# Kernel tuning notes

Hardware: AMD Instinct MI355X
Metric: run time of the kernel (lower is better)

## Reference

```python
import jax, jax.numpy as jnp
import numpy as np

B, S, D, H, DH, FF = 2, 2048, 1024, 16, 64, 4096
EPS = 1e-6


def setup_inputs() -> dict:
    key = jax.random.key(0)
    ks = jax.random.split(key, 12)
    s = lambda fan: 1.0 / np.sqrt(fan)
    return {
        "x": jax.random.normal(ks[0], (B, S, D), dtype=jnp.float32),
        "mask": jax.random.randint(ks[1], (B, S), 0, 2).astype(bool),
        "Wq": jax.random.normal(ks[2], (D, H * DH), dtype=jnp.float32) * s(D),
        "Wk": jax.random.normal(ks[3], (D, H * DH), dtype=jnp.float32) * s(D),
        "Wv": jax.random.normal(ks[4], (D, H * DH), dtype=jnp.float32) * s(D),
        "Wo": jax.random.normal(ks[5], (H * DH, D), dtype=jnp.float32) * s(H * DH),
        "bo": jnp.zeros((D,), dtype=jnp.float32),
        "W1": jax.random.normal(ks[6], (D, FF), dtype=jnp.float32) * s(D),
        "b1": jnp.zeros((FF,), dtype=jnp.float32),
        "W2": jax.random.normal(ks[7], (FF, D), dtype=jnp.float32) * s(FF),
        "b2": jnp.zeros((D,), dtype=jnp.float32),
        "g1": jnp.ones((D,), dtype=jnp.float32),   # layer_norm1 target_std
        "m1": jnp.zeros((D,), dtype=jnp.float32),  # layer_norm1 target_mean
        "g2": jnp.ones((D,), dtype=jnp.float32),
        "m2": jnp.zeros((D,), dtype=jnp.float32),
    }


def layer_norm(x, g, m):
    mu = jnp.mean(x, axis=-1, keepdims=True)
    xc = x - mu
    std = jnp.sqrt(jnp.mean(xc * xc, axis=-1, keepdims=True) + EPS)
    return g * xc / std + m


def reference(x, mask, Wq, Wk, Wv, Wo, bo, W1, b1, W2, b2, g1, m1, g2, m2):
    # --- multi-head self-attention (no proj bias) ---
    q = (x @ Wq).reshape(B, S, H, DH)
    k = (x @ Wk).reshape(B, S, H, DH)
    v = (x @ Wv).reshape(B, S, H, DH)
    scores = jnp.einsum("bqhd,bkhd->bhqk", q, k) / np.sqrt(DH)  # [B,H,S,S]
    scores = jnp.where(mask[:, None, None, :], -jnp.inf, scores)
    att = jax.nn.softmax(scores, axis=-1)
    ctx = jnp.einsum("bhqk,bkhd->bqhd", att, v).reshape(B, S, H * DH)
    attn_out = ctx @ Wo + bo
    # --- post-LN residual block (pre_ln=False, dropouts=0 in eval) ---
    x1 = layer_norm(attn_out + x, g1, m1)
    ff = jax.nn.relu(x1 @ W1 + b1) @ W2 + b2
    return layer_norm(ff + x1, g2, m2)
```

## Files before the change

kernel.cpp:

```cpp
#include <hip/hip_runtime.h>
#include <hip/hip_bf16.h>


typedef __bf16 bf16;
typedef __bf16 bf16x8 __attribute__((ext_vector_type(8)));
typedef __bf16 bf16x4 __attribute__((ext_vector_type(4)));
typedef float  f32x4  __attribute__((ext_vector_type(4)));
typedef float  f32x16 __attribute__((ext_vector_type(16)));
typedef unsigned u32x2 __attribute__((ext_vector_type(2)));
typedef unsigned u32x4 __attribute__((ext_vector_type(4)));

#define DEVI __device__ __forceinline__

constexpr int S_LEN  = 2048;
constexpr int NTOK   = 4096;
constexpr int DMODEL = 1024;
constexpr int NFF    = 4096;
constexpr float SCALE2 = 0.125f * 1.44269504088896f;
constexpr float MASKV2 = -30000.0f;

DEVI void gld16(const void* g, void* l) {
  __builtin_amdgcn_global_load_lds((const __attribute__((address_space(1))) void*)g,
                                   (__attribute__((address_space(3))) void*)l, 16, 0, 0);
}

DEVI f32x4 mfma16(bf16x8 a, bf16x8 b, f32x4 c) {
  return __builtin_amdgcn_mfma_f32_16x16x32_bf16(a, b, c, 0, 0, 0);
}
DEVI f32x16 mfma32(bf16x8 a, bf16x8 b, f32x16 c) {
  return __builtin_amdgcn_mfma_f32_32x32x16_bf16(a, b, c, 0, 0, 0);
}
DEVI unsigned cvtpk(float lo, float hi) {
  unsigned d;
  asm("v_cvt_pk_bf16_f32 %0, %1, %2" : "=v"(d) : "v"(lo), "v"(hi));
  return d;
}
DEVI void plswap(unsigned &a, unsigned &b) {
#if __has_builtin(__builtin_amdgcn_permlane32_swap)
  u32x2 r = __builtin_amdgcn_permlane32_swap(a, b, false, false);
  a = r[0]; b = r[1];
#else
  asm volatile("v_permlane32_swap_b32 %0, %1" : "+v"(a), "+v"(b));
#endif
}
DEVI float fexp2(float x) {
#if __has_builtin(__builtin_amdgcn_exp2f)
  return __builtin_amdgcn_exp2f(x);
#else
  return exp2f(x);
#endif
}
#define M3(a, b, c) fmaxf(fmaxf(a, b), c)

template <int MODE>
__global__ __launch_bounds__(256) void gemm_bt(
    const bf16* __restrict__ A, const bf16* __restrict__ Bt,
    void* __restrict__ out, const float* __restrict__ bias,
    int M, int N, int ld, int Kc, int nx, int ny)
{
  __shared__ bf16 As[128 * 32];
  __shared__ bf16 Bs[128 * 32];
  const int tid  = threadIdx.x;
  const int lane = tid & 63, w = tid >> 6;
  const int wr = w >> 1, wc = w & 1;

  const int id  = blockIdx.x;
  const int xcd = id & 7;
  int t2 = id >> 3;
  const int bx = t2 % nx;  t2 /= nx;
  const int ppx = ny >> 3;
  const int kz = t2 / ppx;
  const int by = xcd * ppx + (t2 % ppx);
  const int brow = by * 128, bcol = bx * 128;

  const bf16* Ag = A  + (size_t)(brow + w * 32 + (lane >> 2)) * ld + kz * Kc + (lane & 3) * 8;
  const bf16* Bg = Bt + (size_t)(bcol + w * 32 + (lane >> 2)) * ld + kz * Kc + (lane & 3) * 8;
  bf16* AsW = As + w * 1024;
  bf16* BsW = Bs + w * 1024;

  f32x4 acc[4][4] = {};

  for (int k0 = 0; k0 < Kc; k0 += 32) {
    gld16(Ag + k0,                    AsW);
    gld16(Ag + k0 + (size_t)16 * ld,  AsW + 512);
    gld16(Bg + k0,                    BsW);
    gld16(Bg + k0 + (size_t)16 * ld,  BsW + 512);
    __syncthreads();

    bf16x8 af[4], bfr[4];
#pragma unroll
    for (int m = 0; m < 4; ++m)
      af[m] = *(const bf16x8*)&As[(wr * 64 + m * 16 + (lane & 15)) * 32 + (lane >> 4) * 8];
#pragma unroll
    for (int n = 0; n < 4; ++n)
      bfr[n] = *(const bf16x8*)&Bs[(wc * 64 + n * 16 + (lane & 15)) * 32 + (lane >> 4) * 8];
    __builtin_amdgcn_s_setprio(1);
#pragma unroll
    for (int m = 0; m < 4; ++m)
#pragma unroll
      for (int n = 0; n < 4; ++n)
        acc[m][n] = mfma16(af[m], bfr[n], acc[m][n]);
    __builtin_amdgcn_s_setprio(0);
    __syncthreads();
  }

  const size_t plane = (size_t)NTOK * DMODEL;
#pragma unroll
  for (int m = 0; m < 4; ++m)
#pragma unroll
    for (int n = 0; n < 4; ++n)
#pragma unroll
      for (int r = 0; r < 4; ++r) {
        const int row = brow + wr * 64 + m * 16 + (lane >> 4) * 4 + r;
        const int col = bcol + wc * 64 + n * 16 + (lane & 15);
        const float v = acc[m][n][r];
        if (MODE == 0) {
          const int b = row >> 11, s = row & 2047;
          const int which = col >> 10, c = col & 1023, h = c >> 6, d = c & 63;
          bf16* qkv = (bf16*)out;
          if (which == 0)
            qkv[(((size_t)(b * 16 + h)) * 2048 + s) * 64 + d] = (bf16)(v * SCALE2);
          else if (which == 1)
            (qkv + plane)[(((size_t)(b * 16 + h)) * 2048 + s) * 64 + d] = (bf16)v;
          else
            (qkv + 2 * plane)[(((size_t)(b * 16 + h)) * 64 + d) * 2048 + s] = (bf16)v;
        } else if (MODE == 3) {
          const float t = v + bias[col];
          ((bf16*)out)[(size_t)row * N + col] = (bf16)fmaxf(t, 0.0f);
        } else {
          ((float*)out)[(size_t)kz * M * N + (size_t)row * N + col] = v;
        }
      }
}

__global__ __launch_bounds__(512) void attn_k(
    const bf16* __restrict__ q, const bf16* __restrict__ k,
    const bf16* __restrict__ vt, const unsigned* __restrict__ mbits,
    bf16* __restrict__ ctx)
{
  __shared__ __align__(16) char smem[36864];
  bf16* Kl = (bf16*)smem;
  bf16* Vl = (bf16*)(smem + 16384);
  const int tid = threadIdx.x, lane = tid & 63, w = tid >> 6;
  const int hi = lane >> 5, li = lane & 31;
  const int id = blockIdx.x;
  const int j = id >> 3;
  const int bh = (id & 7) * 4 + (j & 3);
  const int b = bh >> 4, h = bh & 15;
  const int qbase = (j >> 2) * 256 + w * 32;

  bf16x8 qf[4];
  {
    const bf16* qp = q + ((size_t)bh * S_LEN + qbase + li) * 64 + hi * 8;
#pragma unroll
    for (int c = 0; c < 4; ++c) qf[c] = *(const bf16x8*)(qp + c * 16);
  }
  const u32x4 onesu = {0x3F803F80u, 0x3F803F80u, 0x3F803F80u, 0x3F803F80u};
  const bf16x8 onesv = __builtin_bit_cast(bf16x8, onesu);

  f32x16 o[2] = {};
  f32x16 acc1 = {};
  float mrun = -3.0e38f;

  const int srow = w * 8 + (lane >> 3);
  const int sslot = (lane & 7) ^ ((srow ^ (srow >> 3)) & 7);
  const bf16* kg = k  + ((size_t)bh * S_LEN + srow) * 64 + sslot * 8;
  const bf16* vg = vt + ((size_t)bh * 64 + srow) * S_LEN + sslot * 8;

  gld16(kg, Kl + w * 512);
  gld16(vg, Vl + w * 512);
  __syncthreads();

  int buf = 0;
  for (int kt = 0; kt < 32; ++kt) {
    const int nb = buf ^ 1;
    if (kt + 1 < 32) {
      gld16(kg + (size_t)(kt + 1) * 4096, Kl + nb * 4096 + w * 512);
      gld16(vg + (kt + 1) * 64,           Vl + nb * 4096 + w * 512);
    }
    const unsigned mw0 = mbits[b * 64 + kt * 2]     >> (hi * 4);
    const unsigned mw1 = mbits[b * 64 + kt * 2 + 1] >> (hi * 4);
    const bf16* Kb = Kl + buf * 4096;
    const bf16* Vb = Vl + buf * 4096;

    float sc[2][16];
#pragma unroll
    for (int kblk = 0; kblk < 2; ++kblk) {
      const int key = kblk * 32 + li;
      const unsigned swb = ((key ^ (key >> 3)) & 7) << 4;
      const char* kr = (const char*)Kb + key * 128;
      f32x16 st = {};
      __builtin_amdgcn_s_setprio(1);
#pragma unroll
      for (int c = 0; c < 4; ++c) {
        const bf16x8 kf = *(const bf16x8*)(kr + ((unsigned)(c * 32 + hi * 16) ^ swb));
        st = mfma32(kf, qf[c], st);
      }
      __builtin_amdgcn_s_setprio(0);
      const unsigned msh = kblk ? mw1 : mw0;
#pragma unroll
      for (int r = 0; r < 16; ++r) {
        const int cb = (r & 3) + 8 * (r >> 2);
        sc[kblk][r] = (msh & (1u << cb)) ? MASKV2 : st[r];
      }
    }

    const float* sf = &sc[0][0];
    float m0[11];
#pragma unroll
    for (int i3 = 0; i3 < 10; ++i3) m0[i3] = M3(sf[i3 * 3], sf[i3 * 3 + 1], sf[i3 * 3 + 2]);
    m0[10] = fmaxf(sf[30], sf[31]);
    float tm = fmaxf(fmaxf(M3(m0[0], m0[1], m0[2]), M3(m0[3], m0[4], m0[5])),
                     fmaxf(M3(m0[6], m0[7], m0[8]), fmaxf(m0[9], m0[10])));
    tm = fmaxf(tm, __shfl_xor(tm, 32, 64));

    if (!__all(tm <= mrun + 11.0f)) {
      const float mnew = fmaxf(mrun, tm);
      const float alpha = fexp2(mrun - mnew);
      mrun = mnew;
      o[0] *= alpha;
      o[1] *= alpha;
      acc1[0] = acc1[0] * alpha;
    }
#pragma unroll
    for (int kblk = 0; kblk < 2; ++kblk)
#pragma unroll
      for (int r = 0; r < 16; ++r)
        sc[kblk][r] = fexp2(sc[kblk][r] - mrun);

    bf16x8 pa[4];
#pragma unroll
    for (int kblk = 0; kblk < 2; ++kblk)
#pragma unroll
      for (int hf = 0; hf < 2; ++hf) {
        unsigned A = cvtpk(sc[kblk][hf * 8 + 0], sc[kblk][hf * 8 + 1]);
        unsigned B = cvtpk(sc[kblk][hf * 8 + 2], sc[kblk][hf * 8 + 3]);
        unsigned C = cvtpk(sc[kblk][hf * 8 + 4], sc[kblk][hf * 8 + 5]);
        unsigned D = cvtpk(sc[kblk][hf * 8 + 6], sc[kblk][hf * 8 + 7]);
        plswap(A, C);
        plswap(B, D);
        const u32x4 t = {A, B, C, D};
        pa[kblk * 2 + hf] = __builtin_bit_cast(bf16x8, t);
      }

#pragma unroll
    for (int dblk = 0; dblk < 2; ++dblk) {
      const int d = dblk * 32 + li;
      const unsigned swb = ((d ^ (d >> 3)) & 7) << 4;
      const char* vr = (const char*)Vb + d * 128;
      __builtin_amdgcn_s_setprio(1);
#pragma unroll
      for (int ch = 0; ch < 4; ++ch) {
        const bf16x8 vf = *(const bf16x8*)(vr + ((unsigned)(ch * 32 + hi * 16) ^ swb));
        o[dblk] = mfma32(vf, pa[ch], o[dblk]);
      }
      __builtin_amdgcn_s_setprio(0);
    }
#pragma unroll
    for (int ch = 0; ch < 4; ++ch) acc1 = mfma32(onesv, pa[ch], acc1);
    __syncthreads();
    buf = nb;
  }

  const float rl = 1.0f / acc1[0];
  char* Ep = smem + w * 4608;
#pragma unroll
  for (int dblk = 0; dblk < 2; ++dblk)
#pragma unroll
    for (int g = 0; g < 4; ++g) {
      const unsigned lo = cvtpk(o[dblk][4 * g + 0] * rl, o[dblk][4 * g + 1] * rl);
      const unsigned hw = cvtpk(o[dblk][4 * g + 2] * rl, o[dblk][4 * g + 3] * rl);
      const int d0 = 8 * g + 4 * hi + 32 * dblk;
      *(unsigned long long*)(Ep + li * 144 + d0 * 2) =
          ((unsigned long long)hw << 32) | (unsigned long long)lo;
    }
#pragma unroll
  for (int i = 0; i < 4; ++i) {
    const int r = (lane >> 3) + 8 * i;
    const bf16x8 vv = *(const bf16x8*)(Ep + r * 144 + (lane & 7) * 16);
    *(bf16x8*)(ctx + ((size_t)b * S_LEN + qbase + r) * DMODEL + h * 64 + (lane & 7) * 8) = vv;
  }
}

template <int NPART, int RB>
__global__ __launch_bounds__(256) void ln_k(
    const float* __restrict__ parts, const float* __restrict__ bias,
    const void* __restrict__ resid, const float* __restrict__ gam,
    const float* __restrict__ bet, float* __restrict__ of, bf16* __restrict__ ob)
{
  const int row = blockIdx.x, t = threadIdx.x;
  float4 v = ((const float4*)(parts + (size_t)row * DMODEL))[t];
#pragma unroll
  for (int p = 1; p < NPART; ++p) {
    const float4 u = ((const float4*)(parts + ((size_t)p * NTOK + row) * DMODEL))[t];
    v.x += u.x; v.y += u.y; v.z += u.z; v.w += u.w;
  }
  {
    const float4 b4 = ((const float4*)bias)[t];
    float4 r4;
    if (RB) {
      const bf16x4 rb = *(const bf16x4*)((const bf16*)resid + (size_t)row * DMODEL + t * 4);
      r4.x = (float)rb[0]; r4.y = (float)rb[1]; r4.z = (float)rb[2]; r4.w = (float)rb[3];
    } else {
      r4 = ((const float4*)((const float*)resid + (size_t)row * DMODEL))[t];
    }
    v.x += b4.x + r4.x; v.y += b4.y + r4.y; v.z += b4.z + r4.z; v.w += b4.w + r4.w;
  }
  float s  = v.x + v.y + v.z + v.w;
  float s2 = v.x * v.x + v.y * v.y + v.z * v.z + v.w * v.w;
#pragma unroll
  for (int off = 1; off < 64; off <<= 1) {
    s  += __shfl_xor(s, off, 64);
    s2 += __shfl_xor(s2, off, 64);
  }
  __shared__ float ps[4], ps2[4];
  if ((t & 63) == 0) { ps[t >> 6] = s; ps2[t >> 6] = s2; }
  __syncthreads();
  s  = ps[0] + ps[1] + ps[2] + ps[3];
  s2 = ps2[0] + ps2[1] + ps2[2] + ps2[3];
  const float mu   = s * (1.f / 1024.f);
  const float var  = fmaxf(s2 * (1.f / 1024.f) - mu * mu, 0.f);
  const float rstd = rsqrtf(var + 1e-6f);
  const float4 g4 = ((const float4*)gam)[t];
  const float4 b4 = ((const float4*)bet)[t];
  float4 ov;
  ov.x = g4.x * (v.x - mu) * rstd + b4.x;
  ov.y = g4.y * (v.y - mu) * rstd + b4.y;
  ov.z = g4.z * (v.z - mu) * rstd + b4.z;
  ov.w = g4.w * (v.w - mu) * rstd + b4.w;
  if (of) ((float4*)(of + (size_t)row * DMODEL))[t] = ov;
  if (ob) {
    const bf16x4 o4 = {(bf16)ov.x, (bf16)ov.y, (bf16)ov.z, (bf16)ov.w};
    *(bf16x4*)(ob + (size_t)row * DMODEL + t * 4) = o4;
  }
}

__global__ __launch_bounds__(256) void prep_k(
    const float* __restrict__ x, const float* __restrict__ Wq,
    const float* __restrict__ Wk, const float* __restrict__ Wv,
    const float* __restrict__ Wo, const float* __restrict__ W1,
    const float* __restrict__ W2, const void* __restrict__ mask,
    bf16* __restrict__ xb, bf16* __restrict__ WqkvT, bf16* __restrict__ WoT,
    bf16* __restrict__ W1T, bf16* __restrict__ W2T, unsigned* __restrict__ mbits)
{
  __shared__ float tile[32][33];
  __shared__ int s_gt1, s_f1;
  const int tid = threadIdx.x;
  const int id = blockIdx.x;

  if (id < 4096) {
    const int i = id * 256 + tid;
    const float4 v = ((const float4*)x)[i];
    const bf16x4 o = {(bf16)v.x, (bf16)v.y, (bf16)v.z, (bf16)v.w};
    *(bf16x4*)(xb + (size_t)i * 4) = o;
    return;
  }
  if (id == 16384) {
    if (tid == 0) { s_gt1 = 0; s_f1 = 0; }
    __syncthreads();
    const unsigned* wds = (const unsigned*)mask;
    int gt1 = 0, f1 = 0;
    for (int i = tid; i < 1024; i += 256) {
      const unsigned xw = wds[i];
      gt1 |= (xw > 1u);
      f1  |= (xw == 0x3F800000u);
    }
    if (gt1) atomicOr(&s_gt1, 1);
    if (f1)  atomicOr(&s_f1, 1);
    __syncthreads();
    const int md = s_f1 ? 2 : (s_gt1 ? 1 : 0);
    if (tid < NTOK / 32) {
      unsigned wd = 0;
      for (int jj = 0; jj < 32; ++jj) {
        const int e = tid * 32 + jj;
        unsigned mv;
        if (md == 1)      mv = (((const unsigned char*)mask)[e] != 0);
        else if (md == 2) mv = (((const float*)mask)[e] != 0.f);
        else              mv = (((const int*)mask)[e] != 0);
        wd |= mv << jj;
      }
      mbits[tid] = wd;
    }
    return;
  }
  const float* src; bf16* dst; int K, N, bx, by;
  if (id < 7168) {
    int s2 = id - 4096; const int wq = s2 >> 10; s2 &= 1023;
    src = wq == 0 ? Wq : (wq == 1 ? Wk : Wv);
    dst = WqkvT + (size_t)wq * DMODEL * DMODEL;
    K = 1024; N = 1024; bx = s2 & 31; by = s2 >> 5;
  } else if (id < 8192) {
    const int s2 = id - 7168;
    src = Wo; dst = WoT; K = 1024; N = 1024; bx = s2 & 31; by = s2 >> 5;
  } else if (id < 12288) {
    const int s2 = id - 8192;
    src = W1; dst = W1T; K = 1024; N = 4096; bx = s2 & 127; by = s2 >> 7;
  } else {
    const int s2 = id - 12288;
    src = W2; dst = W2T; K = 4096; N = 1024; bx = s2 & 31; by = s2 >> 5;
  }
  const int tx = tid & 31, ty = tid >> 5;
  const int r0 = by * 32, c0 = bx * 32;
#pragma unroll
  for (int i = 0; i < 32; i += 8)
    tile[ty + i][tx] = src[(size_t)(r0 + ty + i) * N + c0 + tx];
  __syncthreads();
#pragma unroll
  for (int i = 0; i < 32; i += 8)
    dst[(size_t)(c0 + ty + i) * K + r0 + tx] = (bf16)tile[tx][ty + i];
}

extern "C" void kernel_launch(void* const* d_in, const int* in_sizes, int n_in,
                              void* d_out, int out_size, void* d_ws, size_t ws_size,
                              hipStream_t stream)
{
  const float* x    = (const float*)d_in[0];
  const void*  mask = d_in[1];
  const float* Wq   = (const float*)d_in[2];
  const float* Wk   = (const float*)d_in[3];
  const float* Wv   = (const float*)d_in[4];
  const float* Wo   = (const float*)d_in[5];
  const float* bo   = (const float*)d_in[6];
  const float* W1   = (const float*)d_in[7];
  const float* b1   = (const float*)d_in[8];
  const float* W2   = (const float*)d_in[9];
  const float* b2   = (const float*)d_in[10];
  const float* g1   = (const float*)d_in[11];
  const float* m1   = (const float*)d_in[12];
  const float* g2   = (const float*)d_in[13];
  const float* m2   = (const float*)d_in[14];

  const size_t plane = (size_t)NTOK * DMODEL;

  char* ws = (char*)d_ws;
  size_t off = 0;
  auto alloc = [&](size_t bytes) {
    char* p = ws + off;
    off += (bytes + 255) & ~(size_t)255;
    return p;
  };
  bf16* xb     = (bf16*)alloc(plane * 2);
  bf16* WqkvT  = (bf16*)alloc((size_t)3 * DMODEL * DMODEL * 2);
  bf16* WoT    = (bf16*)alloc((size_t)DMODEL * DMODEL * 2);
  bf16* W1T    = (bf16*)alloc((size_t)NFF * DMODEL * 2);
  bf16* W2T    = (bf16*)alloc((size_t)DMODEL * NFF * 2);
  bf16* qkv    = (bf16*)alloc(4 * plane * 2);
  bf16* qb = qkv, *kb = qkv + plane, *vtb = qkv + 2 * plane, *ctxb = qkv + 3 * plane;
  bf16* hb     = qkv;
  float* parts = (float*)alloc(2 * plane * 4);
  bf16*  x1b   = (bf16*)alloc(plane * 2);
  unsigned* maskbits = (unsigned*)alloc(512);

  prep_k<<<dim3(16385), dim3(256), 0, stream>>>(
      x, Wq, Wk, Wv, Wo, W1, W2, mask, xb, WqkvT, WoT, W1T, W2T, maskbits);

  gemm_bt<0><<<dim3(768), dim3(256), 0, stream>>>(
      xb, WqkvT, qkv, nullptr, NTOK, 3 * DMODEL, DMODEL, DMODEL, 24, 32);

  attn_k<<<dim3(256), dim3(512), 0, stream>>>(qb, kb, vtb, maskbits, ctxb);

  gemm_bt<4><<<dim3(512), dim3(256), 0, stream>>>(
      ctxb, WoT, parts, nullptr, NTOK, DMODEL, DMODEL, DMODEL / 2, 8, 32);
  ln_k<2, 0><<<dim3(NTOK), dim3(256), 0, stream>>>(parts, bo, x, g1, m1, nullptr, x1b);

  gemm_bt<3><<<dim3(1024), dim3(256), 0, stream>>>(
      x1b, W1T, hb, b1, NTOK, NFF, DMODEL, DMODEL, 32, 32);
  gemm_bt<4><<<dim3(512), dim3(256), 0, stream>>>(
      hb, W2T, parts, nullptr, NTOK, DMODEL, NFF, NFF / 2, 8, 32);
  ln_k<2, 1><<<dim3(NTOK), dim3(256), 0, stream>>>(parts, b2, x1b, g2, m2, (float*)d_out, nullptr);
}
```

Measured before the change: 271.9 us.

## Add 256x256 eight-wave pipelined GEMM for QKV and FFN1 projections

Adds a new GEMM kernel with 256x256 block tiles, 512 threads, and a 64-wide K step. It double-buffers LDS through direct global-to-LDS loads, swizzles LDS to avoid bank conflicts, and splits each K step into eight phases that interleave the next stage's loads with MFMA work, using explicit vmcnt waits and barriers. The kernel replaces the 128x128 gemm_bt for the QKV projection and the W1+ReLU projection. This targets more reuse per tile and hidden load latency, but uses 128KB of LDS, which limits occupancy to one block per CU. The QKV launch has only 192 blocks, which may leave some CUs idle.

```diff
diff --git a/kernel.cpp b/kernel.cpp
--- a/kernel.cpp
+++ b/kernel.cpp
@@ -51,6 +51,134 @@
 #endif
 }
 #define M3(a, b, c) fmaxf(fmaxf(a, b), c)
+
+template <int MODE>
+__global__ __launch_bounds__(512) void gemm8p(
+    const bf16* __restrict__ A, const bf16* __restrict__ Bt,
+    void* __restrict__ out, const float* __restrict__ bias, int N, int nx)
+{
+  __shared__ bf16 lds8[65536];
+  const int tid = threadIdx.x, lane = tid & 63, w = tid >> 6;
+  const int wr = w >> 2, wc = w & 3;
+  const int li16 = lane & 15, hi4 = lane >> 4, l7 = lane & 7, b3 = (lane >> 3) & 1;
+
+  const int id = blockIdx.x;
+  const int t2 = id >> 3;
+  const int bx = t2 % nx;
+  const int by = (id & 7) * 2 + t2 / nx;
+  const int brow = by * 256, bcol = bx * 256;
+
+  const int srow = tid >> 3;
+  const int ssl  = (tid & 7) ^ ((srow ^ (srow >> 3)) & 7);
+  const bf16* aG = A  + ((size_t)(brow + srow)) * 1024 + ssl * 8;
+  const bf16* bG = Bt + ((size_t)(bcol + srow)) * 1024 + ssl * 8;
+
+  auto STA = [&](int buf, int t, int h) {
+    const bf16* g = aG + t * 64 + (size_t)(h * 2) * 65536;
+    gld16(g,         lds8 + buf * 32768 + (h * 2) * 4096 + w * 512);
+    gld16(g + 65536, lds8 + buf * 32768 + (h * 2 + 1) * 4096 + w * 512);
+  };
+  auto STB = [&](int buf, int t, int h) {
+    const bf16* g = bG + t * 64 + (size_t)(h * 2) * 65536;
+    gld16(g,         lds8 + buf * 32768 + 16384 + (h * 2) * 4096 + w * 512);
+    gld16(g + 65536, lds8 + buf * 32768 + 16384 + (h * 2 + 1) * 4096 + w * 512);
+  };
+
+  const int sa[4] = { l7 ^ ((0 + b3) & 7), l7 ^ ((2 + b3) & 7),
+                      l7 ^ ((4 + b3) & 7), l7 ^ ((6 + b3) & 7) };
+  const int sb[2] = { l7 ^ ((wc * 4 + 0 + b3) & 7), l7 ^ ((wc * 4 + 2 + b3) & 7) };
+
+  f32x4 acc[2][2][4][2] = {};
+
+#define VM4 asm volatile("s_waitcnt vmcnt(4)" ::: "memory")
+#define VM0 asm volatile("s_waitcnt vmcnt(0)" ::: "memory")
+#define NOP ((void)0)
+#define PH(BUF, MQ, NQ, STG, WAIT) do {                                          \
+    bf16x8 af[4][2], bg[2][2];                                                   \
+    _Pragma("unroll") for (int m = 0; m < 4; ++m) {                              \
+      const bf16* rp = lds8 + (BUF) * 32768 +                                    \
+                       ((MQ) * 128 + wr * 64 + m * 16 + li16) * 64;              \
+      _Pragma("unroll") for (int ks = 0; ks < 2; ++ks)                           \
+        af[m][ks] = *(const bf16x8*)(rp + ((ks * 4 + hi4) ^ sa[m]) * 8);         \
+    }                                                                            \
+    _Pragma("unroll") for (int n = 0; n < 2; ++n) {                              \
+      const bf16* rp = lds8 + (BUF) * 32768 + 16384 +                            \
+                       ((NQ) * 128 + wc * 32 + n * 16 + li16) * 64;              \
+      _Pragma("unroll") for (int ks = 0; ks < 2; ++ks)                           \
+        bg[n][ks] = *(const bf16x8*)(rp + ((ks * 4 + hi4) ^ sb[n]) * 8);         \
+    }                                                                            \
+    STG;                                                                         \
+    asm volatile("s_barrier" ::: "memory");                                      \
+    __builtin_amdgcn_s_setprio(1);                                               \
+    _Pragma("unroll") for (int m = 0; m < 4; ++m)                                \
+      _Pragma("unroll") for (int n = 0; n < 2; ++n)                              \
+        _Pragma("unroll") for (int ks = 0; ks < 2; ++ks)                         \
+          acc[MQ][NQ][m][n] = mfma16(af[m][ks], bg[n][ks], acc[MQ][NQ][m][n]);   \
+    __builtin_amdgcn_s_setprio(0);                                               \
+    __builtin_amdgcn_sched_barrier(0);                                           \
+    WAIT;                                                                        \
+    asm volatile("s_barrier" ::: "memory");                                      \
+  } while (0)
+
+  STA(0, 0, 0); STA(0, 0, 1); STB(0, 0, 0); STB(0, 0, 1);
+  STA(1, 1, 0); STB(1, 1, 0);
+  VM4;
+  asm volatile("s_barrier" ::: "memory");
+
+  for (int it = 0; it < 7; ++it) {
+    const int t = 2 * it;
+    PH(0, 0, 0, STA(1, t + 1, 1), NOP);
+    PH(0, 0, 1, STB(1, t + 1, 1), NOP);
+    PH(0, 1, 0, STA(0, t + 2, 0), NOP);
+    PH(0, 1, 1, STB(0, t + 2, 0), VM4);
+    PH(1, 0, 0, STA(0, t + 2, 1), NOP);
+    PH(1, 0, 1, STB(0, t + 2, 1), NOP);
+    PH(1, 1, 0, STA(1, t + 3, 0), NOP);
+    PH(1, 1, 1, STB(1, t + 3, 0), VM4);
+  }
+  PH(0, 0, 0, STA(1, 15, 1), NOP);
+  PH(0, 0, 1, STB(1, 15, 1), NOP);
+  PH(0, 1, 0, NOP, NOP);
+  PH(0, 1, 1, NOP, VM0);
+  PH(1, 0, 0, NOP, NOP);
+  PH(1, 0, 1, NOP, NOP);
+  PH(1, 1, 0, NOP, NOP);
+  PH(1, 1, 1, NOP, NOP);
+#undef PH
+#undef VM4
+#undef VM0
+#undef NOP
+
+  const size_t plane = (size_t)NTOK * DMODEL;
+#pragma unroll
+  for (int mq = 0; mq < 2; ++mq)
+#pragma unroll
+    for (int nq = 0; nq < 2; ++nq)
+#pragma unroll
+      for (int m = 0; m < 4; ++m)
+#pragma unroll
+        for (int n = 0; n < 2; ++n)
+#pragma unroll
+          for (int j = 0; j < 4; ++j) {
+            const int row = brow + mq * 128 + wr * 64 + m * 16 + hi4 * 4 + j;
+            const int col = bcol + nq * 128 + wc * 32 + n * 16 + li16;
+            const float v = acc[mq][nq][m][n][j];
+            if (MODE == 3) {
+              const float t = v + bias[col];
+              ((bf16*)out)[(size_t)row * N + col] = (bf16)fmaxf(t, 0.0f);
+            } else {
+              const int b = row >> 11, s = row & 2047;
+              const int which = col >> 10, c = col & 1023, h = c >> 6, d = c & 63;
+              bf16* qkv = (bf16*)out;
+              if (which == 0)
+                qkv[(((size_t)(b * 16 + h)) * 2048 + s) * 64 + d] = (bf16)(v * SCALE2);
+              else if (which == 1)
+                (qkv + plane)[(((size_t)(b * 16 + h)) * 2048 + s) * 64 + d] = (bf16)v;
+              else
+                (qkv + 2 * plane)[(((size_t)(b * 16 + h)) * 64 + d) * 2048 + s] = (bf16)v;
+            }
+          }
+}
 
 template <int MODE>
 __global__ __launch_bounds__(256) void gemm_bt(
@@ -104,7 +232,6 @@
     __syncthreads();
   }
 
-  const size_t plane = (size_t)NTOK * DMODEL;
 #pragma unroll
   for (int m = 0; m < 4; ++m)
 #pragma unroll
@@ -113,23 +240,7 @@
       for (int r = 0; r < 4; ++r) {
         const int row = brow + wr * 64 + m * 16 + (lane >> 4) * 4 + r;
         const int col = bcol + wc * 64 + n * 16 + (lane & 15);
-        const float v = acc[m][n][r];
-        if (MODE == 0) {
-          const int b = row >> 11, s = row & 2047;
-          const int which = col >> 10, c = col & 1023, h = c >> 6, d = c & 63;
-          bf16* qkv = (bf16*)out;
-          if (which == 0)
-            qkv[(((size_t)(b * 16 + h)) * 2048 + s) * 64 + d] = (bf16)(v * SCALE2);
-          else if (which == 1)
-            (qkv + plane)[(((size_t)(b * 16 + h)) * 2048 + s) * 64 + d] = (bf16)v;
-          else
-            (qkv + 2 * plane)[(((size_t)(b * 16 + h)) * 64 + d) * 2048 + s] = (bf16)v;
-        } else if (MODE == 3) {
-          const float t = v + bias[col];
-          ((bf16*)out)[(size_t)row * N + col] = (bf16)fmaxf(t, 0.0f);
-        } else {
-          ((float*)out)[(size_t)kz * M * N + (size_t)row * N + col] = v;
-        }
+        ((float*)out)[(size_t)kz * M * N + (size_t)row * N + col] = acc[m][n][r];
       }
 }
 
@@ -454,8 +565,7 @@
   prep_k<<<dim3(16385), dim3(256), 0, stream>>>(
       x, Wq, Wk, Wv, Wo, W1, W2, mask, xb, WqkvT, WoT, W1T, W2T, maskbits);
 
-  gemm_bt<0><<<dim3(768), dim3(256), 0, stream>>>(
-      xb, WqkvT, qkv, nullptr, NTOK, 3 * DMODEL, DMODEL, DMODEL, 24, 32);
+  gemm8p<0><<<dim3(192), dim3(512), 0, stream>>>(xb, WqkvT, qkv, nullptr, 3 * DMODEL, 12);
 
   attn_k<<<dim3(256), dim3(512), 0, stream>>>(qb, kb, vtb, maskbits, ctxb);
 
@@ -463,8 +573,7 @@
       ctxb, WoT, parts, nullptr, NTOK, DMODEL, DMODEL, DMODEL / 2, 8, 32);
   ln_k<2, 0><<<dim3(NTOK), dim3(256), 0, stream>>>(parts, bo, x, g1, m1, nullptr, x1b);
 
-  gemm_bt<3><<<dim3(1024), dim3(256), 0, stream>>>(
-      x1b, W1T, hb, b1, NTOK, NFF, DMODEL, DMODEL, 32, 32);
+  gemm8p<3><<<dim3(256), dim3(512), 0, stream>>>(x1b, W1T, hb, b1, NFF, 16);
   gemm_bt<4><<<dim3(512), dim3(256), 0, stream>>>(
       hb, W2T, parts, nullptr, NTOK, DMODEL, NFF, NFF / 2, 8, 32);
   ln_k<2, 1><<<dim3(NTOK), dim3(256), 0, stream>>>(parts, b2, x1b, g2, m2, (float*)d_out, nullptr);
```

Result: slower. 286.0 us (+5.2%).
